# Performance work log

Measured on AMD Instinct MI355X. Metric: run time of the kernel, lower is better.

Reference implementation:

```python
import jax, jax.numpy as jnp
import numpy as np

EMB_DIM = 16

def _pos_enc_table(side_len, emb_dim):
    pos = np.arange(side_len)[:, None].astype(np.float64)
    j = np.arange(emb_dim)[None, :]
    enc = pos / np.power(10000.0, 2.0 * (j // 2) / emb_dim)
    enc[0, :] = 0.0
    enc[1:, 0::2] = np.sin(enc[1:, 0::2])
    enc[1:, 1::2] = np.cos(enc[1:, 1::2])
    return enc.astype(np.float32)  # [L, E]

def _pos_embeddings(side_len, emb_dim):
    t = _pos_enc_table(side_len, emb_dim)
    # original uses raw .view (row-major reshape), NOT a transpose
    x = np.tile(t.reshape(1, emb_dim, side_len, 1), (1, 1, 1, side_len))
    y = np.tile(t.reshape(1, emb_dim, 1, side_len), (1, 1, side_len, 1))
    return jnp.asarray(np.concatenate((x, y), axis=1))  # [1, 2E, L, L]

def setup_inputs() -> dict:
    key = jax.random.key(0)
    ks = jax.random.split(key, 7)
    B, C, L = 32, 224, 32
    Cin = C + 2 * EMB_DIM  # 256
    K = V = 256
    s = 0.02
    return {
        "x": jax.random.normal(ks[0], (B, C, L, L), dtype=jnp.float32),
        "wq": jax.random.normal(ks[1], (K, Cin), dtype=jnp.float32) * s,
        "bq": jax.random.normal(ks[2], (K,), dtype=jnp.float32) * s,
        "wk": jax.random.normal(ks[3], (K, Cin), dtype=jnp.float32) * s,
        "bk": jax.random.normal(ks[4], (K,), dtype=jnp.float32) * s,
        "wv": jax.random.normal(ks[5], (V, Cin), dtype=jnp.float32) * s,
        "bv": jax.random.normal(ks[6], (V,), dtype=jnp.float32) * s,
    }

def reference(x, wq, bq, wk, bk, wv, bv):
    B, C, H, W = x.shape
    S = H * W
    Kdim = wq.shape[0]
    Vdim = wv.shape[0]
    pe = _pos_embeddings(H, EMB_DIM).astype(x.dtype)  # [1, 2E, H, W]
    x0 = jnp.concatenate([x, jnp.broadcast_to(pe, (B, 2 * EMB_DIM, H, W))], axis=1)
    x0 = x0.reshape(B, C + 2 * EMB_DIM, S)  # [B, Cin, S]
    # 1x1 conv == channel matmul, then ReLU nonlin
    q = jax.nn.relu(jnp.einsum('kc,bcs->bks', wq, x0) + bq[None, :, None])
    k = jax.nn.relu(jnp.einsum('kc,bcs->bks', wk, x0) + bk[None, :, None])
    v = jax.nn.relu(jnp.einsum('vc,bcs->bvs', wv, x0) + bv[None, :, None])
    attn = jnp.einsum('bks,bkt->bst', q, k) / jnp.sqrt(jnp.asarray(Kdim, x.dtype))
    mask = jnp.tril(jnp.ones((S, S), dtype=x.dtype))  # causal incl. self
    attn = attn * mask + (1.0 - mask) * (-10000.0)
    attn = jax.nn.softmax(attn, axis=-1) * mask  # double masking as in source
    out1 = jnp.einsum('bst,bvt->bvs', attn, v)  # [B, V, S]
    # NOTE: source computes out1 + fc(out1) but then overwrites with out1.view(...)
    return out1.reshape(B, Vdim, H, W)
```

## Files before the change

### kernel.cpp

```cpp
#include <hip/hip_runtime.h>
#include <cstdint>

typedef float  f32x4  __attribute__((ext_vector_type(4)));
typedef short  short8 __attribute__((ext_vector_type(8)));
typedef _Float16 half4 __attribute__((ext_vector_type(4)));
typedef _Float16 half8 __attribute__((ext_vector_type(8)));

__device__ __forceinline__ unsigned short f2bf(float f) {
    unsigned u = __builtin_bit_cast(unsigned, f);
    u += 0x7FFFu + ((u >> 16) & 1u);
    return (unsigned short)(u >> 16);
}

__global__ void wconv_kernel(const float* __restrict__ wq,
                             const float* __restrict__ wk,
                             const float* __restrict__ wv,
                             unsigned short* __restrict__ Wb) {
    int p = blockIdx.x >> 8;
    int i = ((blockIdx.x & 255) << 8) + threadIdx.x;
    const float* src = (p == 0) ? wq : ((p == 1) ? wk : wv);
    Wb[(p << 16) + i] = f2bf(src[i]);
}

__global__ __launch_bounds__(256, 2) void fproj_kernel(
        const float* __restrict__ x,
        const unsigned short* __restrict__ Wb,
        const float* __restrict__ bq, const float* __restrict__ bk,
        const float* __restrict__ bv,
        unsigned short* __restrict__ Q, unsigned short* __restrict__ K,
        _Float16* __restrict__ V) {
    __shared__ __align__(16) char Xlds[32768];
    __shared__ __align__(16) char Wlds[32768];
    float* Tt = (float*)Wlds;

    int st = blockIdx.x;
    int b  = blockIdx.y;
    int sb = st << 6;
    int tid = threadIdx.x; int w = tid >> 6; int l = tid & 63;
    int g = l >> 4, c = l & 15;
    int wr = w >> 1, wc = w & 1;

    #pragma unroll 1
    for (int sc = 0; sc < 2; ++sc) {
        if (sc) __syncthreads();
        #pragma unroll
        for (int r = 0; r < 28; ++r) {
            int idx = r * 256 + tid;
            int cc = idx >> 5, lo = idx & 31;
            Tt[cc * 33 + lo] = x[((b * 224 + cc) << 10) + sb + (sc << 5) + lo];
        }
        __syncthreads();
        #pragma unroll
        for (int r = 0; r < 4; ++r) {
            int idx = r * 256 + tid;
            if (idx < 896) {
                int cc16 = idx >> 5;
                int sl = idx & 31;
                int s = (sc << 5) + sl;
                short8 v8;
                #pragma unroll
                for (int j = 0; j < 8; ++j)
                    v8[j] = (short)f2bf(Tt[(cc16 * 8 + j) * 33 + sl]);
                *(short8*)&Xlds[(s << 9) + ((cc16 ^ (s & 7)) << 4)] = v8;
            }
        }
        if (tid < 128) {
            int sl = tid >> 2;
            int cc16 = 28 + (tid & 3);
            int s = (sc << 5) + sl;
            int sg = sb + s;
            int h = sg >> 5, ww = sg & 31;
            short8 v8;
            #pragma unroll
            for (int j = 0; j < 8; ++j) {
                int ch = (cc16 - 28) * 8 + j;
                int i = (ch < 16) ? (ch * 32 + h) : ((ch - 16) * 32 + ww);
                int ll = i >> 4, e = i & 15;
                float val = 0.f;
                if (ll > 0) {
                    float ang = (float)ll * powf(10000.f, -(float)(e >> 1) * 0.125f);
                    val = (e & 1) ? cosf(ang) : sinf(ang);
                }
                v8[j] = (short)f2bf(val);
            }
            *(short8*)&Xlds[(s << 9) + ((cc16 ^ (s & 7)) << 4)] = v8;
        }
    }
    __syncthreads();

    short8 af[2][8];
    #pragma unroll
    for (int i = 0; i < 2; ++i) {
        const char* ab = &Xlds[(wr * 32 + i * 16 + c) << 9];
        #pragma unroll
        for (int kk = 0; kk < 8; ++kk)
            af[i][kk] = *(const short8*)&ab[((kk * 4 + g) ^ (c & 7)) << 4];
    }

    #pragma unroll 1
    for (int pj = 0; pj < 3; ++pj) {
        const float* bias = (pj == 0) ? bq : ((pj == 1) ? bk : bv);
        #pragma unroll 1
        for (int ot = 0; ot < 4; ++ot) {
            const unsigned short* Wg = Wb + (pj << 16) + (ot << 14);
            #pragma unroll
            for (int p = 0; p < 8; ++p) {
                int ch = p * 256 + tid;
                int row = ch >> 5;
                int cl = (ch & 31) ^ (row & 7);
                __builtin_amdgcn_global_load_lds(
                    (const unsigned int*)&Wg[(row << 8) + cl * 8],
                    (unsigned int*)(Wlds + ((p << 8) + (w << 6)) * 16), 16, 0, 0);
            }
            asm volatile("s_waitcnt vmcnt(0)\n\ts_barrier" ::: "memory");

            f32x4 acc[2][2];
            #pragma unroll
            for (int i = 0; i < 2; ++i)
                #pragma unroll
                for (int j = 0; j < 2; ++j) acc[i][j] = (f32x4){0.f, 0.f, 0.f, 0.f};

            const char* bb0 = &Wlds[(wc * 32 + c) << 9];
            const char* bb1 = &Wlds[(wc * 32 + 16 + c) << 9];
            __builtin_amdgcn_s_setprio(1);
            #pragma unroll
            for (int kk = 0; kk < 8; ++kk) {
                int co = ((kk * 4 + g) ^ (c & 7)) << 4;
                short8 b0 = *(const short8*)&bb0[co];
                short8 b1 = *(const short8*)&bb1[co];
                acc[0][0] = __builtin_amdgcn_mfma_f32_16x16x32_bf16(af[0][kk], b0, acc[0][0], 0, 0, 0);
                acc[0][1] = __builtin_amdgcn_mfma_f32_16x16x32_bf16(af[0][kk], b1, acc[0][1], 0, 0, 0);
                acc[1][0] = __builtin_amdgcn_mfma_f32_16x16x32_bf16(af[1][kk], b0, acc[1][0], 0, 0, 0);
                acc[1][1] = __builtin_amdgcn_mfma_f32_16x16x32_bf16(af[1][kk], b1, acc[1][1], 0, 0, 0);
            }
            __builtin_amdgcn_s_setprio(0);

            #pragma unroll
            for (int j = 0; j < 2; ++j) {
                int o = (ot << 6) + wc * 32 + j * 16 + c;
                float bbv = bias[o];
                #pragma unroll
                for (int i = 0; i < 2; ++i) {
                    int sgb = sb + wr * 32 + i * 16;
                    if (pj < 2) {
                        unsigned short* dst = (pj == 0) ? Q : K;
                        #pragma unroll
                        for (int r = 0; r < 4; ++r) {
                            float v = fmaxf(acc[i][j][r] + bbv, 0.f);
                            int s = sgb + 4 * g + r;
                            dst[(((b << 10) + s) << 8) + o] = f2bf(v);
                        }
                    } else {
                        half4 hv;
                        #pragma unroll
                        for (int r = 0; r < 4; ++r)
                            hv[r] = (_Float16)fmaxf(acc[i][j][r] + bbv, 0.f);
                        int hi = (sgb >> 4) & 1;
                        int tt = sgb >> 5;
                        *(half4*)&V[((size_t)((b << 5) + tt) << 13)
                                    + ((o << 2) + (g ^ ((o >> 1) & 3))) * 8
                                    + (hi << 2)] = hv;
                    }
                }
            }
            __syncthreads();
        }
    }
}

__global__ __launch_bounds__(256, 2) void attn_kernel(
        const unsigned short* __restrict__ Q,
        const unsigned short* __restrict__ K,
        const _Float16* __restrict__ V,
        float* __restrict__ out) {
    __shared__ __align__(16) char Klds[2][16384];
    __shared__ __align__(16) char Vlds[2][16384];

    int bid = blockIdx.x;
    int xcd  = bid & 7;
    int qv   = (bid >> 3) & 7;
    int bhi  = (bid >> 6) & 3;
    int hf   = bid >> 8;
    int b  = (bhi << 3) | xcd;
    int qt = hf ? qv : (15 - qv);

    int tid = threadIdx.x; int w = tid >> 6; int l = tid & 63;
    int g = l >> 4, c = l & 15;
    int s0 = (qt << 6) + (w << 4);

    short8 qf[8];
    #pragma unroll
    for (int kk = 0; kk < 8; ++kk)
        qf[kk] = *(const short8*)&Q[(((b << 10) + s0 + c) << 8) + kk * 32 + g * 8];

    float m = -1e30f, lsum = 0.f;
    f32x4 acc[16];
    #pragma unroll
    for (int i = 0; i < 16; ++i) acc[i] = (f32x4){0.f, 0.f, 0.f, 0.f};

    const unsigned short* Kb_ = &K[(size_t)b << 18];
    const _Float16*       Vb_ = &V[(size_t)b << 18];

    int nt = 2 * qt + 2;
    int dt = 2 * qt + (w >> 1);

    auto stage = [&](int t, int bufi) {
        int t0 = t << 5;
        #pragma unroll
        for (int j = 0; j < 4; ++j) {
            int ch = (j << 8) + tid;
            int trow = ch >> 5;
            int cl = (ch & 31) ^ (trow & 7);
            __builtin_amdgcn_global_load_lds(
                (const unsigned int*)&Kb_[((t0 + trow) << 8) + cl * 8],
                (unsigned int*)(Klds[bufi] + ((j << 8) + (w << 6)) * 16), 16, 0, 0);
        }
        #pragma unroll
        for (int j = 0; j < 4; ++j) {
            int ch = (j << 8) + tid;
            __builtin_amdgcn_global_load_lds(
                (const unsigned int*)&Vb_[((size_t)t << 13) + ch * 8],
                (unsigned int*)(Vlds[bufi] + ((j << 8) + (w << 6)) * 16), 16, 0, 0);
        }
    };

    stage(0, 0);

    for (int t = 0; t < nt; ++t) {
        asm volatile("s_waitcnt vmcnt(0)\n\ts_barrier" ::: "memory");
        if (t + 1 < nt) stage(t + 1, (t + 1) & 1);
        if (t > dt) continue;

        const char* Kl = Klds[t & 1];
        const char* Vl = Vlds[t & 1];
        half8 vread[16];
        #pragma unroll
        for (int vt = 0; vt < 16; ++vt) {
            int pos = (vt << 6) + (c << 2) + (g ^ ((c >> 1) & 3));
            vread[vt] = *(const half8*)&Vl[pos << 4];
        }
        #pragma unroll
        for (int sub = 0; sub < 2; ++sub) {
            bool dmask = (t == dt) && (sub == (w & 1));
            if ((t == dt) && !(w & 1) && sub == 1) break;
            int toff = sub << 4;
            f32x4 sc0 = {0.f,0.f,0.f,0.f}, sc1 = {0.f,0.f,0.f,0.f};
            const char* kbase = &Kl[(toff + c) * 512];
            __builtin_amdgcn_s_setprio(1);
            #pragma unroll
            for (int kk = 0; kk < 8; kk += 2) {
                short8 a0 = *(const short8*)&kbase[(((kk * 4 + g)       ^ (c & 7)) << 4)];
                short8 a1 = *(const short8*)&kbase[((((kk + 1) * 4 + g) ^ (c & 7)) << 4)];
                sc0 = __builtin_amdgcn_mfma_f32_16x16x32_bf16(a0, qf[kk], sc0, 0, 0, 0);
                sc1 = __builtin_amdgcn_mfma_f32_16x16x32_bf16(a1, qf[kk + 1], sc1, 0, 0, 0);
            }
            __builtin_amdgcn_s_setprio(0);
            float sv[4];
            #pragma unroll
            for (int r = 0; r < 4; ++r) sv[r] = (sc0[r] + sc1[r]) * 0.0625f;
            if (dmask) {
                #pragma unroll
                for (int r = 0; r < 4; ++r)
                    if (4 * g + r > c) sv[r] = -1e30f;
            }
            float tm = fmaxf(fmaxf(sv[0], sv[1]), fmaxf(sv[2], sv[3]));
            if (!__all((int)(tm <= m + 8.f))) {
                float tr = fmaxf(tm, __shfl_xor(tm, 16));
                tr = fmaxf(tr, __shfl_xor(tr, 32));
                float mnew = fmaxf(m, tr);
                float alpha = __expf(m - mnew);
                m = mnew;
                lsum *= alpha;
                #pragma unroll
                for (int i = 0; i < 16; ++i) acc[i] *= alpha;
            }
            float p[4];
            #pragma unroll
            for (int r = 0; r < 4; ++r) { p[r] = __expf(sv[r] - m); lsum += p[r]; }
            half4 pb;
            #pragma unroll
            for (int r = 0; r < 4; ++r) pb[r] = (_Float16)p[r];
            __builtin_amdgcn_s_setprio(1);
            #pragma unroll
            for (int vt = 0; vt < 16; ++vt) {
                half4 vf;
                #pragma unroll
                for (int jj = 0; jj < 4; ++jj) vf[jj] = vread[vt][sub * 4 + jj];
                acc[vt] = __builtin_amdgcn_mfma_f32_16x16x16f16(vf, pb, acc[vt], 0, 0, 0);
            }
            __builtin_amdgcn_s_setprio(0);
        }
    }

    lsum += __shfl_xor(lsum, 16);
    lsum += __shfl_xor(lsum, 32);
    float rl = 1.f / lsum;
    #pragma unroll
    for (int vt = 0; vt < 16; ++vt) {
        #pragma unroll
        for (int r = 0; r < 4; ++r)
            out[(((b << 8) + vt * 16 + 4 * g + r) << 10) + s0 + c] = acc[vt][r] * rl;
    }
}

extern "C" void kernel_launch(void* const* d_in, const int* in_sizes, int n_in,
                              void* d_out, int out_size, void* d_ws, size_t ws_size,
                              hipStream_t stream) {
    const float* x  = (const float*)d_in[0];
    const float* wq = (const float*)d_in[1];
    const float* bq = (const float*)d_in[2];
    const float* wk = (const float*)d_in[3];
    const float* bk = (const float*)d_in[4];
    const float* wv = (const float*)d_in[5];
    const float* bv = (const float*)d_in[6];
    float* out = (float*)d_out;

    char* ws = (char*)d_ws;
    unsigned short* Wb = (unsigned short*)ws;
    unsigned short* Qb = (unsigned short*)(ws + 393216);
    unsigned short* Kb = (unsigned short*)(ws + 393216 + 16777216);
    _Float16*       Vb = (_Float16*)     (ws + 393216 + 2 * 16777216);

    wconv_kernel<<<768, 256, 0, stream>>>(wq, wk, wv, Wb);
    fproj_kernel<<<dim3(16, 32), 256, 0, stream>>>(x, Wb, bq, bk, bv, Qb, Kb, Vb);
    attn_kernel<<<512, 256, 0, stream>>>(Qb, Kb, Vb, out);
}
```

Before: 99.65 us.

## Switch attention to 32x32 MFMA with split-KV across wave pairs and LDS merge

The attention kernel moves from 16x16 MFMA tiles to 32x32x16 MFMA, with each wave now handling 32 query rows. Pairs of waves split the key tiles by parity and merge their partial softmax states through LDS at the end. The V layout swizzle in the projection kernel changes to match the new fragment reads. The aim is higher MFMA throughput and fewer LDS fragment reads per flop, at the cost of cross-lane shuffles to form P fragments, an extra LDS-based reduction, and more accumulator registers.

```diff
diff --git a/kernel.cpp b/kernel.cpp
--- a/kernel.cpp
+++ b/kernel.cpp
@@ -2,14 +2,20 @@
 #include <cstdint>
 
 typedef float  f32x4  __attribute__((ext_vector_type(4)));
+typedef float  f32x16 __attribute__((ext_vector_type(16)));
 typedef short  short8 __attribute__((ext_vector_type(8)));
 typedef _Float16 half4 __attribute__((ext_vector_type(4)));
 typedef _Float16 half8 __attribute__((ext_vector_type(8)));
+typedef _Float16 half2v __attribute__((ext_vector_type(2)));
 
 __device__ __forceinline__ unsigned short f2bf(float f) {
     unsigned u = __builtin_bit_cast(unsigned, f);
     u += 0x7FFFu + ((u >> 16) & 1u);
     return (unsigned short)(u >> 16);
+}
+
+__device__ __forceinline__ half2v pkrtz(float a, float b) {
+    return __builtin_bit_cast(half2v, __builtin_amdgcn_cvt_pkrtz(a, b));
 }
 
 __global__ void wconv_kernel(const float* __restrict__ wq,
@@ -157,9 +163,9 @@
                             hv[r] = (_Float16)fmaxf(acc[i][j][r] + bbv, 0.f);
                         int hi = (sgb >> 4) & 1;
                         int tt = sgb >> 5;
+                        int ci = ((hi << 1) | (g >> 1)) ^ ((o >> 1) & 3);
                         *(half4*)&V[((size_t)((b << 5) + tt) << 13)
-                                    + ((o << 2) + (g ^ ((o >> 1) & 3))) * 8
-                                    + (hi << 2)] = hv;
+                                    + ((o << 2) + ci) * 8 + ((g & 1) << 2)] = hv;
                     }
                 }
             }
@@ -175,6 +181,7 @@
         float* __restrict__ out) {
     __shared__ __align__(16) char Klds[2][16384];
     __shared__ __align__(16) char Vlds[2][16384];
+    __shared__ float cml[2][2][64];
 
     int bid = blockIdx.x;
     int xcd  = bid & 7;
@@ -185,24 +192,29 @@
     int qt = hf ? qv : (15 - qv);
 
     int tid = threadIdx.x; int w = tid >> 6; int l = tid & 63;
-    int g = l >> 4, c = l & 15;
-    int s0 = (qt << 6) + (w << 4);
-
-    short8 qf[8];
+    int lo = l >> 5, cs = l & 31;
+    int sh = w >> 1, par = w & 1;
+    int s0 = (qt << 6) + (sh << 5);
+    int sg = s0 + cs;
+
+    short8 qf[16];
+    const unsigned short* Qrow = &Q[(((b << 10) + s0 + cs) << 8) + lo * 8];
     #pragma unroll
-    for (int kk = 0; kk < 8; ++kk)
-        qf[kk] = *(const short8*)&Q[(((b << 10) + s0 + c) << 8) + kk * 32 + g * 8];
-
+    for (int kc = 0; kc < 16; ++kc)
+        qf[kc] = *(const short8*)&Qrow[kc * 16];
+
+    f32x16 acc[8];
+    #pragma unroll
+    for (int i = 0; i < 8; ++i)
+        #pragma unroll
+        for (int r = 0; r < 16; ++r) acc[i][r] = 0.f;
     float m = -1e30f, lsum = 0.f;
-    f32x4 acc[16];
-    #pragma unroll
-    for (int i = 0; i < 16; ++i) acc[i] = (f32x4){0.f, 0.f, 0.f, 0.f};
 
     const unsigned short* Kb_ = &K[(size_t)b << 18];
     const _Float16*       Vb_ = &V[(size_t)b << 18];
 
     int nt = 2 * qt + 2;
-    int dt = 2 * qt + (w >> 1);
+    int dtile = 2 * qt + sh;
 
     auto stage = [&](int t, int bufi) {
         int t0 = t << 5;
@@ -229,77 +241,130 @@
     for (int t = 0; t < nt; ++t) {
         asm volatile("s_waitcnt vmcnt(0)\n\ts_barrier" ::: "memory");
         if (t + 1 < nt) stage(t + 1, (t + 1) & 1);
-        if (t > dt) continue;
+        if (((t & 1) != par) || t > dtile) continue;
 
         const char* Kl = Klds[t & 1];
         const char* Vl = Vlds[t & 1];
-        half8 vread[16];
-        #pragma unroll
-        for (int vt = 0; vt < 16; ++vt) {
-            int pos = (vt << 6) + (c << 2) + (g ^ ((c >> 1) & 3));
-            vread[vt] = *(const half8*)&Vl[pos << 4];
-        }
-        #pragma unroll
-        for (int sub = 0; sub < 2; ++sub) {
-            bool dmask = (t == dt) && (sub == (w & 1));
-            if ((t == dt) && !(w & 1) && sub == 1) break;
-            int toff = sub << 4;
-            f32x4 sc0 = {0.f,0.f,0.f,0.f}, sc1 = {0.f,0.f,0.f,0.f};
-            const char* kbase = &Kl[(toff + c) * 512];
+        int t0 = t << 5;
+        f32x16 sc0, sc1;
+        #pragma unroll
+        for (int r = 0; r < 16; ++r) { sc0[r] = 0.f; sc1[r] = 0.f; }
+        __builtin_amdgcn_s_setprio(1);
+        #pragma unroll
+        for (int kc = 0; kc < 16; kc += 2) {
+            int p0 = (cs << 5) + (((kc << 1) | lo) ^ (cs & 7));
+            int p1 = (cs << 5) + ((((kc + 1) << 1) | lo) ^ (cs & 7));
+            short8 a0 = *(const short8*)&Kl[p0 << 4];
+            short8 a1 = *(const short8*)&Kl[p1 << 4];
+            sc0 = __builtin_amdgcn_mfma_f32_32x32x16_bf16(a0, qf[kc], sc0, 0, 0, 0);
+            sc1 = __builtin_amdgcn_mfma_f32_32x32x16_bf16(a1, qf[kc + 1], sc1, 0, 0, 0);
+        }
+        __builtin_amdgcn_s_setprio(0);
+        bool diag = (t == dtile);
+        float sv[16];
+        #pragma unroll
+        for (int r = 0; r < 16; ++r) {
+            sv[r] = (sc0[r] + sc1[r]) * 0.0625f;
+            if (diag) {
+                int tg = t0 + (r & 3) + 8 * (r >> 2) + 4 * lo;
+                if (tg > sg) sv[r] = -1e30f;
+            }
+        }
+        float tm = sv[0];
+        #pragma unroll
+        for (int r = 1; r < 16; ++r) tm = fmaxf(tm, sv[r]);
+        if (!__all((int)(tm <= m + 8.f))) {
+            float tr = fmaxf(tm, __shfl_xor(tm, 32));
+            float mnew = fmaxf(m, tr);
+            float alpha = __expf(m - mnew);
+            m = mnew;
+            lsum *= alpha;
+            #pragma unroll
+            for (int i = 0; i < 8; ++i)
+                #pragma unroll
+                for (int r = 0; r < 16; ++r) acc[i][r] *= alpha;
+        }
+        float p[16];
+        #pragma unroll
+        for (int r = 0; r < 16; ++r) { p[r] = __expf(sv[r] - m); lsum += p[r]; }
+        half2v ph[8];
+        #pragma unroll
+        for (int i = 0; i < 8; ++i)
+            ph[i] = pkrtz(p[2 * i], p[2 * i + 1]);
+        {
+            half2v po[4];
+            #pragma unroll
+            for (int i = 0; i < 4; ++i)
+                po[i] = __builtin_bit_cast(half2v,
+                    __shfl_xor(__builtin_bit_cast(int, ph[i]), 32));
+            half2v e0 = lo ? po[2] : ph[0];
+            half2v e1 = lo ? po[3] : ph[1];
+            half2v e2 = lo ? ph[2] : po[0];
+            half2v e3 = lo ? ph[3] : po[1];
+            half8 frag = {e0[0], e0[1], e1[0], e1[1], e2[0], e2[1], e3[0], e3[1]};
             __builtin_amdgcn_s_setprio(1);
             #pragma unroll
-            for (int kk = 0; kk < 8; kk += 2) {
-                short8 a0 = *(const short8*)&kbase[(((kk * 4 + g)       ^ (c & 7)) << 4)];
-                short8 a1 = *(const short8*)&kbase[((((kk + 1) * 4 + g) ^ (c & 7)) << 4)];
-                sc0 = __builtin_amdgcn_mfma_f32_16x16x32_bf16(a0, qf[kk], sc0, 0, 0, 0);
-                sc1 = __builtin_amdgcn_mfma_f32_16x16x32_bf16(a1, qf[kk + 1], sc1, 0, 0, 0);
+            for (int vt = 0; vt < 8; ++vt) {
+                int v = (vt << 5) + cs;
+                int pos = (v << 2) + (lo ^ ((v >> 1) & 3));
+                half8 vf = *(const half8*)&Vl[pos << 4];
+                acc[vt] = __builtin_amdgcn_mfma_f32_32x32x16_f16(vf, frag, acc[vt], 0, 0, 0);
             }
             __builtin_amdgcn_s_setprio(0);
-            float sv[4];
-            #pragma unroll
-            for (int r = 0; r < 4; ++r) sv[r] = (sc0[r] + sc1[r]) * 0.0625f;
-            if (dmask) {
-                #pragma unroll
-                for (int r = 0; r < 4; ++r)
-                    if (4 * g + r > c) sv[r] = -1e30f;
-            }
-            float tm = fmaxf(fmaxf(sv[0], sv[1]), fmaxf(sv[2], sv[3]));
-            if (!__all((int)(tm <= m + 8.f))) {
-                float tr = fmaxf(tm, __shfl_xor(tm, 16));
-                tr = fmaxf(tr, __shfl_xor(tr, 32));
-                float mnew = fmaxf(m, tr);
-                float alpha = __expf(m - mnew);
-                m = mnew;
-                lsum *= alpha;
-                #pragma unroll
-                for (int i = 0; i < 16; ++i) acc[i] *= alpha;
-            }
-            float p[4];
-            #pragma unroll
-            for (int r = 0; r < 4; ++r) { p[r] = __expf(sv[r] - m); lsum += p[r]; }
-            half4 pb;
-            #pragma unroll
-            for (int r = 0; r < 4; ++r) pb[r] = (_Float16)p[r];
+        }
+        {
+            half2v po[4];
+            #pragma unroll
+            for (int i = 0; i < 4; ++i)
+                po[i] = __builtin_bit_cast(half2v,
+                    __shfl_xor(__builtin_bit_cast(int, ph[4 + i]), 32));
+            half2v e0 = lo ? po[2] : ph[4];
+            half2v e1 = lo ? po[3] : ph[5];
+            half2v e2 = lo ? ph[6] : po[0];
+            half2v e3 = lo ? ph[7] : po[1];
+            half8 frag = {e0[0], e0[1], e1[0], e1[1], e2[0], e2[1], e3[0], e3[1]};
             __builtin_amdgcn_s_setprio(1);
             #pragma unroll
-            for (int vt = 0; vt < 16; ++vt) {
-                half4 vf;
-                #pragma unroll
-                for (int jj = 0; jj < 4; ++jj) vf[jj] = vread[vt][sub * 4 + jj];
-                acc[vt] = __builtin_amdgcn_mfma_f32_16x16x16f16(vf, pb, acc[vt], 0, 0, 0);
+            for (int vt = 0; vt < 8; ++vt) {
+                int v = (vt << 5) + cs;
+                int pos = (v << 2) + ((2 | lo) ^ ((v >> 1) & 3));
+                half8 vf = *(const half8*)&Vl[pos << 4];
+                acc[vt] = __builtin_amdgcn_mfma_f32_32x32x16_f16(vf, frag, acc[vt], 0, 0, 0);
             }
             __builtin_amdgcn_s_setprio(0);
         }
     }
 
-    lsum += __shfl_xor(lsum, 16);
-    lsum += __shfl_xor(lsum, 32);
-    float rl = 1.f / lsum;
-    #pragma unroll
-    for (int vt = 0; vt < 16; ++vt) {
-        #pragma unroll
-        for (int r = 0; r < 4; ++r)
-            out[(((b << 8) + vt * 16 + 4 * g + r) << 10) + s0 + c] = acc[vt][r] * rl;
+    __syncthreads();
+    float* cb = sh ? (float*)Vlds : (float*)Klds;
+    if (par == 1) {
+        #pragma unroll
+        for (int i = 0; i < 8; ++i)
+            #pragma unroll
+            for (int r = 0; r < 16; ++r)
+                cb[((i * 16 + r) << 6) + l] = acc[i][r];
+        cml[sh][0][l] = m;
+        cml[sh][1][l] = lsum;
+    }
+    __syncthreads();
+    if (par == 0) {
+        float m1 = cml[sh][0][l];
+        float l1 = cml[sh][1][l];
+        float ms = fmaxf(m, m1);
+        float a0 = __expf(m - ms);
+        float a1 = __expf(m1 - ms);
+        float lt = lsum * a0 + l1 * a1;
+        lt += __shfl_xor(lt, 32);
+        float rl = 1.f / lt;
+        #pragma unroll
+        for (int i = 0; i < 8; ++i) {
+            #pragma unroll
+            for (int r = 0; r < 16; ++r) {
+                float vv = (acc[i][r] * a0 + cb[((i * 16 + r) << 6) + l] * a1) * rl;
+                int vrow = (i << 5) + (r & 3) + 8 * (r >> 2) + 4 * lo;
+                out[(((b << 8) + vrow) << 10) + sg] = vv;
+            }
+        }
     }
 }
 
```

Result: slower. 296.5 us (+197.6%).
